# Kernel optimization log

Hardware: AMD Instinct MI355X
Metric: run time of the kernel (lower is better)

The kernel has to match this reference:

```python
import jax, jax.numpy as jnp
import numpy as np

D_MODEL = 1024
D_INNER = 2048
D_STATE = 16
DT_RANK = 64
D_CONV = 4
EPS = 1e-5
B_SZ, L = 2, 2048


def setup_inputs() -> dict:
    key = jax.random.key(0)
    ks = jax.random.split(key, 8)
    s = 0.02
    inp = {
        "x": jax.random.normal(ks[0], (B_SZ, L, D_MODEL), jnp.float32),
        "in_proj_w": jax.random.normal(ks[1], (D_MODEL, 2 * D_INNER), jnp.float32) * s,
        "conv_w": jax.random.normal(ks[2], (D_INNER, 1, D_CONV), jnp.float32) * s,
        "conv_b": jnp.zeros((D_INNER,), jnp.float32),
        "x_proj_w": jax.random.normal(ks[3], (D_INNER, DT_RANK + 2 * D_STATE), jnp.float32) * s,
        "dt_proj_w": jax.random.normal(ks[4], (DT_RANK, D_INNER), jnp.float32) * s,
        "dt_proj_b": jax.random.normal(ks[5], (D_INNER,), jnp.float32) * s,
        "A_log": jnp.log(jnp.broadcast_to(jnp.arange(1, D_STATE + 1, dtype=jnp.float32), (D_INNER, D_STATE))),
        "D": jnp.ones((D_INNER,), jnp.float32),
        "out_proj_w": jax.random.normal(ks[6], (D_INNER, D_MODEL), jnp.float32) * s,
        "norm_w": jnp.ones((D_MODEL,), jnp.float32),
    }
    return inp


def _silu(x):
    return x * jax.nn.sigmoid(x)


def reference(x, in_proj_w, conv_w, conv_b, x_proj_w, dt_proj_w, dt_proj_b,
              A_log, D, out_proj_w, norm_w):
    b, l, d = x.shape
    # RMSNorm
    xn = x * jax.lax.rsqrt(jnp.mean(x * x, axis=-1, keepdims=True) + EPS) * norm_w
    # in_proj -> split into x branch and residual (gate) branch
    x_and_res = xn @ in_proj_w                      # (b, l, 2*d_inner)
    xi, res = jnp.split(x_and_res, 2, axis=-1)
    # causal depthwise conv1d (pad left d_conv-1, equivalent to torch pad+truncate)
    xc = jax.lax.conv_general_dilated(
        xi.transpose(0, 2, 1),                      # (b, d_inner, l)
        conv_w,                                     # (d_inner, 1, d_conv) = OIH
        window_strides=(1,),
        padding=[(D_CONV - 1, 0)],
        feature_group_count=D_INNER,
        dimension_numbers=("NCH", "OIH", "NCH"),
    ) + conv_b[None, :, None]
    xi = _silu(xc.transpose(0, 2, 1))               # (b, l, d_inner)
    # SSM parameters
    x_dbl = xi @ x_proj_w                           # (b, l, dt_rank + 2n)
    delta, Bm, Cm = jnp.split(x_dbl, [DT_RANK, DT_RANK + D_STATE], axis=-1)
    delta = jax.nn.softplus(delta @ dt_proj_w + dt_proj_b)   # (b, l, d_inner)
    A = -jnp.exp(A_log)                             # (d_inner, n)
    # discretize
    deltaA = jnp.exp(delta[..., None] * A)                          # (b,l,d,n)
    deltaB_u = delta[..., None] * Bm[:, :, None, :] * xi[..., None]  # (b,l,d,n)
    # selective scan over sequence length via lax.scan
    def step(state, inputs):
        dA_t, dBu_t, C_t = inputs                   # (b,d,n),(b,d,n),(b,n)
        state = dA_t * state + dBu_t
        y_t = jnp.einsum("bdn,bn->bd", state, C_t)
        return state, y_t
    state0 = jnp.zeros((b, D_INNER, D_STATE), xi.dtype)
    _, ys = jax.lax.scan(
        step, state0,
        (deltaA.transpose(1, 0, 2, 3), deltaB_u.transpose(1, 0, 2, 3), Cm.transpose(1, 0, 2)),
    )                                               # ys: (l, b, d_inner)
    y = ys.transpose(1, 0, 2) + xi * D              # skip connection D*u
    y = y * _silu(res)                              # gate
    out = y @ out_proj_w + x                        # out_proj + residual add
    return out
```

## Files before the change

### kernel.cpp

```cpp
#include <hip/hip_runtime.h>
#include <cstdint>

#define D_MODEL 1024
#define D_INNER 2048
#define NSTATE  16
#define DT_RANK 64
#define SEQ     2048
#define NBATCH  2
#define NTOK    (NBATCH * SEQ)

#define NC      32
#define CHK     64
#define NGRP    8

typedef float  f32x4  __attribute__((ext_vector_type(4)));
typedef __bf16 bf16x8 __attribute__((ext_vector_type(8)));
typedef short  s16x8  __attribute__((ext_vector_type(8)));

__device__ __forceinline__ unsigned short f2bf(float f) {
  union { float f; uint32_t u; } a; a.f = f;
  uint32_t u = a.u;
  uint32_t r = (u + 0x7FFFu + ((u >> 16) & 1u)) >> 16;
  return (unsigned short)r;
}
__device__ __forceinline__ float bf2f(unsigned short h) {
  union { uint32_t u; float f; } a; a.u = ((uint32_t)h) << 16;
  return a.f;
}

__device__ __forceinline__ void gload16(const void* g, void* l) {
  __builtin_amdgcn_global_load_lds((__attribute__((address_space(1))) void*)g,
                                   (__attribute__((address_space(3))) void*)l,
                                   16, 0, 0);
}

__global__ __launch_bounds__(256) void rmsnorm_kernel(const float* __restrict__ x,
                                                      const float* __restrict__ nw,
                                                      unsigned short* __restrict__ xn) {
  const int row = blockIdx.x;
  const float4 v = ((const float4*)(x + (size_t)row * D_MODEL))[threadIdx.x];
  float ss = v.x*v.x + v.y*v.y + v.z*v.z + v.w*v.w;
  #pragma unroll
  for (int m = 32; m; m >>= 1) ss += __shfl_xor(ss, m);
  __shared__ float red[4];
  if ((threadIdx.x & 63) == 0) red[threadIdx.x >> 6] = ss;
  __syncthreads();
  const float tot = red[0] + red[1] + red[2] + red[3];
  const float rs = rsqrtf(tot * (1.0f / D_MODEL) + 1e-5f);
  const float4 w = ((const float4*)nw)[threadIdx.x];
  ushort4 o;
  o.x = f2bf(v.x * rs * w.x);
  o.y = f2bf(v.y * rs * w.y);
  o.z = f2bf(v.z * rs * w.z);
  o.w = f2bf(v.w * rs * w.w);
  ((ushort4*)(xn + (size_t)row * D_MODEL))[threadIdx.x] = o;
}

__global__ __launch_bounds__(256) void transpose_cast_kernel(const float* __restrict__ W,
                                                             unsigned short* __restrict__ Wt,
                                                             int K, int N, int Npad) {
  __shared__ float tile[32][33];
  const int tx = threadIdx.x & 31, ty = threadIdx.x >> 5;
  const int kt = blockIdx.y * 32, nt = blockIdx.x * 32;
  #pragma unroll
  for (int i = 0; i < 4; ++i) {
    const int k = kt + ty + i*8, n = nt + tx;
    tile[ty + i*8][tx] = (k < K && n < N) ? W[(size_t)k * N + n] : 0.0f;
  }
  __syncthreads();
  #pragma unroll
  for (int i = 0; i < 4; ++i) {
    const int n = nt + ty + i*8, k = kt + tx;
    if (n < Npad && k < K) Wt[(size_t)n * K + k] = f2bf(tile[tx][ty + i*8]);
  }
}

template<int MODE>
__device__ __forceinline__ void gemm_body(const unsigned short* __restrict__ A,
                                          const unsigned short* __restrict__ Bt,
                                          const int M, const int N, const int K,
                                          void* __restrict__ out0,
                                          void* __restrict__ out1,
                                          const float* __restrict__ extra) {
  __shared__ __align__(16) unsigned short sA[128 * 32];
  __shared__ __align__(16) unsigned short sB[128 * 32];
  const int tid = threadIdx.x;
  const int w = tid >> 6, lane = tid & 63;
  const int m0 = blockIdx.y * 128, n0 = blockIdx.x * 128;
  const int wm = w >> 1, wn = w & 1;
  const int lr = lane & 15, kq = lane >> 4;

  f32x4 acc[4][4] = {};

  const int r0 = tid >> 2;
  const int qb = ((tid & 3) ^ (r0 & 3)) * 16;
  const char* pA0 = (const char*)A + ((size_t)(m0 + r0)      * K) * 2 + qb;
  const char* pA1 = (const char*)A + ((size_t)(m0 + r0 + 64) * K) * 2 + qb;
  const char* pB0 = (const char*)Bt + ((size_t)(n0 + r0)      * K) * 2 + qb;
  const char* pB1 = (const char*)Bt + ((size_t)(n0 + r0 + 64) * K) * 2 + qb;
  char* ldsA0 = (char*)sA + w * 1024;
  char* ldsA1 = (char*)sA + 4096 + w * 1024;
  char* ldsB0 = (char*)sB + w * 1024;
  char* ldsB1 = (char*)sB + 4096 + w * 1024;

  const int kqs = (kq ^ (lr & 3)) * 8;
  const unsigned short* pa = sA + (wm*64 + lr) * 32 + kqs;
  const unsigned short* pb = sB + (wn*64 + lr) * 32 + kqs;

  for (int k0 = 0; k0 < K; k0 += 32) {
    __syncthreads();
    gload16(pA0 + (size_t)k0 * 2, ldsA0);
    gload16(pA1 + (size_t)k0 * 2, ldsA1);
    gload16(pB0 + (size_t)k0 * 2, ldsB0);
    gload16(pB1 + (size_t)k0 * 2, ldsB1);
    __syncthreads();
    bf16x8 af[4], bb[4];
    #pragma unroll
    for (int mf = 0; mf < 4; ++mf)
      af[mf] = __builtin_bit_cast(bf16x8, *(const s16x8*)(pa + mf * 16 * 32));
    #pragma unroll
    for (int nf = 0; nf < 4; ++nf)
      bb[nf] = __builtin_bit_cast(bf16x8, *(const s16x8*)(pb + nf * 16 * 32));
    #pragma unroll
    for (int mf = 0; mf < 4; ++mf)
      #pragma unroll
      for (int nf = 0; nf < 4; ++nf)
        acc[mf][nf] = __builtin_amdgcn_mfma_f32_16x16x32_bf16(af[mf], bb[nf], acc[mf][nf], 0, 0, 0);
  }

  #pragma unroll
  for (int mf = 0; mf < 4; ++mf) {
    #pragma unroll
    for (int nf = 0; nf < 4; ++nf) {
      #pragma unroll
      for (int r = 0; r < 4; ++r) {
        const int row = m0 + wm*64 + mf*16 + kq*4 + r;
        const int col = n0 + wn*64 + nf*16 + lr;
        const float v = acc[mf][nf][r];
        if constexpr (MODE == 0) {
          if (col < D_INNER) ((unsigned short*)out0)[(size_t)row * D_INNER + col] = f2bf(v);
          else               ((unsigned short*)out1)[(size_t)row * D_INNER + (col - D_INNER)] = f2bf(v);
        } else if constexpr (MODE == 1) {
          if (col < DT_RANK) ((unsigned short*)out0)[(size_t)row * DT_RANK + col] = f2bf(v);
          else if (col < DT_RANK + 2*NSTATE) ((float*)out1)[(size_t)row * (2*NSTATE) + (col - DT_RANK)] = v;
        } else if constexpr (MODE == 2) {
          const float t = v + extra[col];
          const float sp = (t > 30.0f) ? t : __logf(1.0f + __expf(t));
          ((unsigned short*)out0)[(size_t)row * D_INNER + col] = f2bf(sp);
        } else {
          ((float*)out0)[(size_t)row * D_MODEL + col] = v + extra[(size_t)row * D_MODEL + col];
        }
      }
    }
  }
}

__global__ __launch_bounds__(256) void g0_inproj_kernel(const unsigned short* A, const unsigned short* Bt,
                                                        int M, int N, int K, void* o0, void* o1, const float* ex) {
  gemm_body<0>(A, Bt, M, N, K, o0, o1, ex);
}
__global__ __launch_bounds__(256) void g1_xproj_kernel(const unsigned short* A, const unsigned short* Bt,
                                                       int M, int N, int K, void* o0, void* o1, const float* ex) {
  gemm_body<1>(A, Bt, M, N, K, o0, o1, ex);
}
__global__ __launch_bounds__(256) void g2_dtproj_kernel(const unsigned short* A, const unsigned short* Bt,
                                                        int M, int N, int K, void* o0, void* o1, const float* ex) {
  gemm_body<2>(A, Bt, M, N, K, o0, o1, ex);
}
__global__ __launch_bounds__(256) void g3_outproj_kernel(const unsigned short* A, const unsigned short* Bt,
                                                         int M, int N, int K, void* o0, void* o1, const float* ex) {
  gemm_body<3>(A, Bt, M, N, K, o0, o1, ex);
}

__global__ __launch_bounds__(256) void conv_silu_kernel(const unsigned short* __restrict__ xi_raw,
                                                        const float* __restrict__ cw,
                                                        const float* __restrict__ cb,
                                                        unsigned short* __restrict__ xi) {
  const int t = blockIdx.x * 256 + threadIdx.x;
  const int d8 = (t & 255) * 8;
  const int row = t >> 8;
  const int l = row & (SEQ - 1);

  float acc[8];
  #pragma unroll
  for (int c = 0; c < 8; c += 4) {
    const f32x4 bv = *(const f32x4*)(cb + d8 + c);
    acc[c+0] = bv[0]; acc[c+1] = bv[1]; acc[c+2] = bv[2]; acc[c+3] = bv[3];
  }
  f32x4 wv[8];
  #pragma unroll
  for (int c = 0; c < 8; ++c) wv[c] = ((const f32x4*)cw)[d8 + c];

  #pragma unroll
  for (int tap = 0; tap < 4; ++tap) {
    const int lp = l - 3 + tap;
    if (lp >= 0) {
      const s16x8 v = *(const s16x8*)(xi_raw + (size_t)(row - 3 + tap) * D_INNER + d8);
      #pragma unroll
      for (int c = 0; c < 8; ++c)
        acc[c] += wv[c][tap] * bf2f((unsigned short)v[c]);
    }
  }
  s16x8 o;
  #pragma unroll
  for (int c = 0; c < 8; ++c) {
    const float a = acc[c] / (1.0f + __expf(-acc[c]));
    o[c] = (short)f2bf(a);
  }
  *(s16x8*)(xi + (size_t)row * D_INNER + d8) = o;
}

template<int PASS>
__global__ __launch_bounds__(256) void scan_pass_kernel(const unsigned short* __restrict__ delta,
                                                        const unsigned short* __restrict__ xi,
                                                        const unsigned short* __restrict__ res,
                                                        const float* __restrict__ BC,
                                                        const float* __restrict__ A_log,
                                                        const float* __restrict__ Dv,
                                                        const float* __restrict__ initS,
                                                        float* __restrict__ aprodOut,
                                                        float* __restrict__ sendOut,
                                                        unsigned short* __restrict__ yg) {
  const int tid = threadIdx.x;
  const int db = blockIdx.x & 7;
  const int c  = (blockIdx.x >> 3) & (NC - 1);
  const int b  = blockIdx.x >> 8;
  const int d  = db * 256 + tid;
  const int row0 = b * SEQ + c * CHK;
  const size_t ob = ((size_t)(b * NC + c) * D_INNER + d) * 16;

  float Ac[16];
  #pragma unroll
  for (int q = 0; q < 4; ++q) {
    f32x4 t = ((const f32x4*)(A_log + (size_t)d * 16))[q];
    Ac[q*4+0] = -expf(t[0]); Ac[q*4+1] = -expf(t[1]);
    Ac[q*4+2] = -expf(t[2]); Ac[q*4+3] = -expf(t[3]);
  }
  float s[16];
  float ap[16];
  if constexpr (PASS == 0) {
    #pragma unroll
    for (int n = 0; n < 16; ++n) { s[n] = 0.0f; ap[n] = 1.0f; }
  } else {
    #pragma unroll
    for (int q = 0; q < 4; ++q)
      ((f32x4*)s)[q] = ((const f32x4*)(initS + ob))[q];
  }
  float Dd = 0.0f;
  if constexpr (PASS == 1) Dd = Dv[d];

  __shared__ float bcbuf[2][8][32];
  auto stageg = [&](int g, int p) {
    bcbuf[p][tid >> 5][tid & 31] = BC[(size_t)(row0 + g * 8) * 32 + tid];
  };
  stageg(0, 0);

  for (int g = 0; g < NGRP; ++g) {
    unsigned short dl[8], uu[8], rr[8];
    #pragma unroll
    for (int j = 0; j < 8; ++j) {
      const size_t row = (size_t)(row0 + g * 8 + j) * D_INNER + d;
      dl[j] = delta[row];
      uu[j] = xi[row];
      if constexpr (PASS == 1) rr[j] = res[row];
    }
    __syncthreads();
    if (g + 1 < NGRP) stageg(g + 1, (g + 1) & 1);

    #pragma unroll
    for (int j = 0; j < 8; ++j) {
      const float dlt = bf2f(dl[j]);
      const float u   = bf2f(uu[j]);
      const float dlu = dlt * u;
      float bc[32];
      #pragma unroll
      for (int q = 0; q < (PASS ? 8 : 4); ++q)
        ((f32x4*)bc)[q] = ((const f32x4*)(&bcbuf[g & 1][j][0]))[q];
      #pragma unroll
      for (int n = 0; n < 16; ++n) {
        const float dA = __expf(dlt * Ac[n]);
        s[n] = dA * s[n] + dlu * bc[n];
        if constexpr (PASS == 0) ap[n] *= dA;
      }
      if constexpr (PASS == 1) {
        float y = 0.0f;
        #pragma unroll
        for (int n = 0; n < 16; ++n) y += s[n] * bc[16 + n];
        const float r = bf2f(rr[j]);
        const float o = (y + u * Dd) * (r / (1.0f + __expf(-r)));
        yg[(size_t)(row0 + g * 8 + j) * D_INNER + d] = f2bf(o);
      }
    }
  }

  if constexpr (PASS == 0) {
    #pragma unroll
    for (int q = 0; q < 4; ++q) {
      ((f32x4*)(aprodOut + ob))[q] = ((f32x4*)ap)[q];
      ((f32x4*)(sendOut + ob))[q]  = ((f32x4*)s)[q];
    }
  }
}

__global__ __launch_bounds__(256) void scan_combine_kernel(const float* __restrict__ aprod,
                                                           const float* __restrict__ send,
                                                           float* __restrict__ initS) {
  const int t = blockIdx.x * 256 + threadIdx.x;
  const int b = t >> 13;
  const int rq = t & 8191;
  f32x4 carry = {0.0f, 0.0f, 0.0f, 0.0f};
  #pragma unroll
  for (int c = 0; c < NC; ++c) {
    const size_t idx = (size_t)(b * NC + c) * 8192 + rq;
    ((f32x4*)initS)[idx] = carry;
    const f32x4 a = ((const f32x4*)aprod)[idx];
    const f32x4 e = ((const f32x4*)send)[idx];
    carry = a * carry + e;
  }
}

extern "C" void kernel_launch(void* const* d_in, const int* in_sizes, int n_in,
                              void* d_out, int out_size, void* d_ws, size_t ws_size,
                              hipStream_t stream) {
  const float* x        = (const float*)d_in[0];
  const float* in_proj  = (const float*)d_in[1];
  const float* conv_w   = (const float*)d_in[2];
  const float* conv_b   = (const float*)d_in[3];
  const float* x_proj   = (const float*)d_in[4];
  const float* dt_proj  = (const float*)d_in[5];
  const float* dt_b     = (const float*)d_in[6];
  const float* A_log    = (const float*)d_in[7];
  const float* Dv       = (const float*)d_in[8];
  const float* out_proj = (const float*)d_in[9];
  const float* norm_w   = (const float*)d_in[10];

  char* ws = (char*)d_ws;
  size_t off = 0;
  auto alloc = [&](size_t bytes) {
    char* p = ws + off; off += (bytes + 255) & ~(size_t)255; return p;
  };
  unsigned short* xn     = (unsigned short*)alloc((size_t)NTOK * D_MODEL * 2);
  unsigned short* W1t    = (unsigned short*)alloc((size_t)(2 * D_INNER) * D_MODEL * 2);
  unsigned short* xi_raw = (unsigned short*)alloc((size_t)NTOK * D_INNER * 2);
  unsigned short* resb   = (unsigned short*)alloc((size_t)NTOK * D_INNER * 2);
  unsigned short* xi     = (unsigned short*)alloc((size_t)NTOK * D_INNER * 2);
  unsigned short* W2t    = (unsigned short*)alloc((size_t)128 * D_INNER * 2);
  unsigned short* dr     = (unsigned short*)alloc((size_t)NTOK * DT_RANK * 2);
  float*          BC     = (float*)alloc((size_t)NTOK * 32 * 4);
  unsigned short* W3t    = (unsigned short*)alloc((size_t)D_INNER * DT_RANK * 2);
  unsigned short* dlt    = (unsigned short*)alloc((size_t)NTOK * D_INNER * 2);
  unsigned short* ygb    = (unsigned short*)alloc((size_t)NTOK * D_INNER * 2);
  unsigned short* W4t    = (unsigned short*)alloc((size_t)D_MODEL * D_INNER * 2);

  float* aprod = (float*)xi_raw;
  float* send  = (float*)((char*)xi_raw + 8388608);
  float* initS = (float*)xn;

  rmsnorm_kernel<<<NTOK, 256, 0, stream>>>(x, norm_w, xn);
  transpose_cast_kernel<<<dim3(4096/32, 1024/32), 256, 0, stream>>>(in_proj, W1t, 1024, 4096, 4096);
  transpose_cast_kernel<<<dim3(128/32, 2048/32), 256, 0, stream>>>(x_proj, W2t, 2048, 96, 128);
  transpose_cast_kernel<<<dim3(2048/32, 64/32), 256, 0, stream>>>(dt_proj, W3t, 64, 2048, 2048);
  transpose_cast_kernel<<<dim3(1024/32, 2048/32), 256, 0, stream>>>(out_proj, W4t, 2048, 1024, 1024);

  g0_inproj_kernel<<<dim3(4096/128, 4096/128), 256, 0, stream>>>(xn, W1t, NTOK, 4096, 1024, xi_raw, resb, nullptr);
  conv_silu_kernel<<<NTOK, 256, 0, stream>>>(xi_raw, conv_w, conv_b, xi);
  g1_xproj_kernel<<<dim3(1, 4096/128), 256, 0, stream>>>(xi, W2t, NTOK, 128, 2048, dr, BC, nullptr);
  g2_dtproj_kernel<<<dim3(2048/128, 4096/128), 256, 0, stream>>>(dr, W3t, NTOK, 2048, 64, dlt, nullptr, dt_b);

  scan_pass_kernel<0><<<NBATCH * NC * (D_INNER/256), 256, 0, stream>>>(
      dlt, xi, nullptr, BC, A_log, nullptr, nullptr, aprod, send, nullptr);
  scan_combine_kernel<<<64, 256, 0, stream>>>(aprod, send, initS);
  scan_pass_kernel<1><<<NBATCH * NC * (D_INNER/256), 256, 0, stream>>>(
      dlt, xi, resb, BC, A_log, Dv, initS, nullptr, nullptr, ygb);

  g3_outproj_kernel<<<dim3(1024/128, 4096/128), 256, 0, stream>>>(ygb, W4t, NTOK, 1024, 2048, d_out, nullptr, x);
}
```

Measured before the change: 378.5 us.

## Double-buffer GEMM LDS tiles and fuse prep kernels into one launch

The GEMM main loop now double-buffers its LDS tiles. It issues the async global-to-LDS loads for the next K-slice before computing the current one, which drops one barrier per iteration and overlaps load latency with MFMA work. The RMSNorm and the four weight transpose-cast kernels are merged into a single launch that picks its role by block index, cutting four kernel launches. The cost is twice the LDS per GEMM block, which may lower occupancy. The single-barrier schedule also depends on the async LDS loads being complete at that barrier.

```diff
diff --git a/kernel.cpp b/kernel.cpp
--- a/kernel.cpp
+++ b/kernel.cpp
@@ -34,15 +34,12 @@
                                    16, 0, 0);
 }
 
-__global__ __launch_bounds__(256) void rmsnorm_kernel(const float* __restrict__ x,
-                                                      const float* __restrict__ nw,
-                                                      unsigned short* __restrict__ xn) {
-  const int row = blockIdx.x;
+__device__ __forceinline__ void rms_body(const float* __restrict__ x, const float* __restrict__ nw,
+                                         unsigned short* __restrict__ xn, int row, float* red) {
   const float4 v = ((const float4*)(x + (size_t)row * D_MODEL))[threadIdx.x];
   float ss = v.x*v.x + v.y*v.y + v.z*v.z + v.w*v.w;
   #pragma unroll
   for (int m = 32; m; m >>= 1) ss += __shfl_xor(ss, m);
-  __shared__ float red[4];
   if ((threadIdx.x & 63) == 0) red[threadIdx.x >> 6] = ss;
   __syncthreads();
   const float tot = red[0] + red[1] + red[2] + red[3];
@@ -56,12 +53,10 @@
   ((ushort4*)(xn + (size_t)row * D_MODEL))[threadIdx.x] = o;
 }
 
-__global__ __launch_bounds__(256) void transpose_cast_kernel(const float* __restrict__ W,
-                                                             unsigned short* __restrict__ Wt,
-                                                             int K, int N, int Npad) {
-  __shared__ float tile[32][33];
+__device__ __forceinline__ void tr_body(const float* __restrict__ W, unsigned short* __restrict__ Wt,
+                                        int K, int N, int Npad, int bx, int by, float (*tile)[33]) {
   const int tx = threadIdx.x & 31, ty = threadIdx.x >> 5;
-  const int kt = blockIdx.y * 32, nt = blockIdx.x * 32;
+  const int kt = by * 32, nt = bx * 32;
   #pragma unroll
   for (int i = 0; i < 4; ++i) {
     const int k = kt + ty + i*8, n = nt + tx;
@@ -72,6 +67,30 @@
   for (int i = 0; i < 4; ++i) {
     const int n = nt + ty + i*8, k = kt + tx;
     if (n < Npad && k < K) Wt[(size_t)n * K + k] = f2bf(tile[tx][ty + i*8]);
+  }
+}
+
+__global__ __launch_bounds__(256) void prep_fused_kernel(const float* x, const float* nw, unsigned short* xn,
+                                                         const float* W1, unsigned short* W1t,
+                                                         const float* W2, unsigned short* W2t,
+                                                         const float* W3, unsigned short* W3t,
+                                                         const float* W4, unsigned short* W4t) {
+  __shared__ float shbuf[32][33];
+  const int b = blockIdx.x;
+  if (b < 4096) {
+    rms_body(x, nw, xn, b, &shbuf[0][0]);
+  } else if (b < 8192) {
+    const int i = b - 4096;
+    tr_body(W1, W1t, 1024, 4096, 4096, i & 127, i >> 7, shbuf);
+  } else if (b < 8448) {
+    const int i = b - 8192;
+    tr_body(W2, W2t, 2048, 96, 128, i & 3, i >> 2, shbuf);
+  } else if (b < 8576) {
+    const int i = b - 8448;
+    tr_body(W3, W3t, 64, 2048, 2048, i & 63, i >> 6, shbuf);
+  } else {
+    const int i = b - 8576;
+    tr_body(W4, W4t, 2048, 1024, 1024, i & 31, i >> 5, shbuf);
   }
 }
 
@@ -82,8 +101,8 @@
                                           void* __restrict__ out0,
                                           void* __restrict__ out1,
                                           const float* __restrict__ extra) {
-  __shared__ __align__(16) unsigned short sA[128 * 32];
-  __shared__ __align__(16) unsigned short sB[128 * 32];
+  __shared__ __align__(16) unsigned short sA[2][128 * 32];
+  __shared__ __align__(16) unsigned short sB[2][128 * 32];
   const int tid = threadIdx.x;
   const int w = tid >> 6, lane = tid & 63;
   const int m0 = blockIdx.y * 128, n0 = blockIdx.x * 128;
@@ -98,22 +117,18 @@
   const char* pA1 = (const char*)A + ((size_t)(m0 + r0 + 64) * K) * 2 + qb;
   const char* pB0 = (const char*)Bt + ((size_t)(n0 + r0)      * K) * 2 + qb;
   const char* pB1 = (const char*)Bt + ((size_t)(n0 + r0 + 64) * K) * 2 + qb;
-  char* ldsA0 = (char*)sA + w * 1024;
-  char* ldsA1 = (char*)sA + 4096 + w * 1024;
-  char* ldsB0 = (char*)sB + w * 1024;
-  char* ldsB1 = (char*)sB + 4096 + w * 1024;
 
   const int kqs = (kq ^ (lr & 3)) * 8;
-  const unsigned short* pa = sA + (wm*64 + lr) * 32 + kqs;
-  const unsigned short* pb = sB + (wn*64 + lr) * 32 + kqs;
-
-  for (int k0 = 0; k0 < K; k0 += 32) {
-    __syncthreads();
-    gload16(pA0 + (size_t)k0 * 2, ldsA0);
-    gload16(pA1 + (size_t)k0 * 2, ldsA1);
-    gload16(pB0 + (size_t)k0 * 2, ldsB0);
-    gload16(pB1 + (size_t)k0 * 2, ldsB1);
-    __syncthreads();
+
+  auto stage = [&](int p, int k0) {
+    gload16(pA0 + (size_t)k0 * 2, (char*)sA[p] + w * 1024);
+    gload16(pA1 + (size_t)k0 * 2, (char*)sA[p] + 4096 + w * 1024);
+    gload16(pB0 + (size_t)k0 * 2, (char*)sB[p] + w * 1024);
+    gload16(pB1 + (size_t)k0 * 2, (char*)sB[p] + 4096 + w * 1024);
+  };
+  auto compute = [&](int p) {
+    const unsigned short* pa = sA[p] + (wm*64 + lr) * 32 + kqs;
+    const unsigned short* pb = sB[p] + (wn*64 + lr) * 32 + kqs;
     bf16x8 af[4], bb[4];
     #pragma unroll
     for (int mf = 0; mf < 4; ++mf)
@@ -126,7 +141,18 @@
       #pragma unroll
       for (int nf = 0; nf < 4; ++nf)
         acc[mf][nf] = __builtin_amdgcn_mfma_f32_16x16x32_bf16(af[mf], bb[nf], acc[mf][nf], 0, 0, 0);
-  }
+  };
+
+  stage(0, 0);
+  __syncthreads();
+  int p = 0;
+  for (int k0 = 32; k0 < K; k0 += 32) {
+    stage(p ^ 1, k0);
+    compute(p);
+    __syncthreads();
+    p ^= 1;
+  }
+  compute(p);
 
   #pragma unroll
   for (int mf = 0; mf < 4; ++mf) {
@@ -356,11 +382,9 @@
   float* send  = (float*)((char*)xi_raw + 8388608);
   float* initS = (float*)xn;
 
-  rmsnorm_kernel<<<NTOK, 256, 0, stream>>>(x, norm_w, xn);
-  transpose_cast_kernel<<<dim3(4096/32, 1024/32), 256, 0, stream>>>(in_proj, W1t, 1024, 4096, 4096);
-  transpose_cast_kernel<<<dim3(128/32, 2048/32), 256, 0, stream>>>(x_proj, W2t, 2048, 96, 128);
-  transpose_cast_kernel<<<dim3(2048/32, 64/32), 256, 0, stream>>>(dt_proj, W3t, 64, 2048, 2048);
-  transpose_cast_kernel<<<dim3(1024/32, 2048/32), 256, 0, stream>>>(out_proj, W4t, 2048, 1024, 1024);
+  prep_fused_kernel<<<10624, 256, 0, stream>>>(x, norm_w, xn,
+                                               in_proj, W1t, x_proj, W2t,
+                                               dt_proj, W3t, out_proj, W4t);
 
   g0_inproj_kernel<<<dim3(4096/128, 4096/128), 256, 0, stream>>>(xn, W1t, NTOK, 4096, 1024, xi_raw, resb, nullptr);
   conv_silu_kernel<<<NTOK, 256, 0, stream>>>(xi_raw, conv_w, conv_b, xi);
```

Measured after the change: 369.1 us. 2.5% less time.
